# Kernel tuning notes

Hardware: AMD Instinct MI355X
Metric: run time of the kernel (lower is better)

## Reference

```python
import jax, jax.numpy as jnp
import numpy as np

KSIZE = 21
SCALE = 4

def _conv1x1(h, w, b):
    # h: (B, Ci, H, W), w: (Co, Ci), b: (Co,)
    return jnp.einsum('oi,bihw->bohw', w, h) + b[None, :, None, None]

def setup_inputs() -> dict:
    key = jax.random.key(0)
    ks = jax.random.split(key, 8)
    B, C, H, W = 16, 3, 256, 256
    in_nc, nf, nb, K2 = 64, 64, 8, KSIZE * KSIZE
    Hl, Wl = H // SCALE, W // SCALE
    wscale = 0.1
    return {
        'x': jax.random.normal(ks[0], (B, C, H, W), jnp.float32),
        'z': jax.random.normal(ks[1], (B, in_nc, Hl, Wl), jnp.float32),
        'w_in': wscale * jax.random.normal(ks[2], (nf, in_nc), jnp.float32),
        'b_in': jnp.zeros((nf,), jnp.float32),
        'res_w1': wscale * jax.random.normal(ks[3], (nb, nf, nf), jnp.float32),
        'res_b1': jnp.zeros((nb, nf), jnp.float32),
        'res_w2': wscale * jax.random.normal(ks[4], (nb, nf, nf), jnp.float32),
        'res_b2': jnp.zeros((nb, nf), jnp.float32),
        'w_out': wscale * jax.random.normal(ks[5], (K2, nf), jnp.float32),
        'b_out': jnp.zeros((K2,), jnp.float32),
    }

def reference(x, z, w_in, b_in, res_w1, res_b1, res_w2, res_b2, w_out, b_out):
    B, C, H, W = x.shape
    Hl, Wl = z.shape[2], z.shape[3]
    K2 = KSIZE * KSIZE
    pad = KSIZE // 2

    # --- kernel prediction trunk (all 1x1 convs) ---
    h = _conv1x1(z, w_in, b_in)
    for i in range(res_w1.shape[0]):  # fixed n_layers loop
        r = _conv1x1(h, res_w1[i], res_b1[i])
        r = _conv1x1(jax.nn.relu(r), res_w2[i], res_b2[i])
        h = h + r
    logits = _conv1x1(h, w_out, b_out)            # (B, K2, Hl, Wl)
    kernel = jax.nn.softmax(logits, axis=1)       # softmax over kernel taps

    # --- reflection pad + unfold (im2col) with stride=scale ---
    xp = jnp.pad(x, ((0, 0), (0, 0), (pad, pad), (pad, pad)), mode='reflect')
    xr = xp.reshape(B * C, 1, H + 2 * pad, W + 2 * pad)
    patches = jax.lax.conv_general_dilated_patches(
        xr, filter_shape=(KSIZE, KSIZE), window_strides=(SCALE, SCALE),
        padding='VALID', dimension_numbers=('NCHW', 'OIHW', 'NCHW'))
    patches = patches.reshape(B, C, K2, Hl, Wl)   # (B, C, K2, Hl, Wl)

    # --- per-pixel spatially-varying kernel apply ---
    out = (patches * kernel[:, None]).sum(axis=2)  # (B, C, Hl, Wl)
    return out, kernel
```

## Files before the change

### kernel.cpp

```cpp
#include <hip/hip_runtime.h>
#include <math.h>

#define KS 21
#define K2 441
#define NB 8
#define PPI 4096
#define NPIX 65536
#define STR 72
#define XW 276
#define BPX 256
#define NTH 1024
#define XROWS 33
#define XRS 2208
#define LOG2E 1.4426950408889634f

typedef unsigned short u16;
typedef unsigned int u32;
typedef short short8v __attribute__((ext_vector_type(8)));
typedef float f32x4 __attribute__((ext_vector_type(4)));
typedef float f32x16 __attribute__((ext_vector_type(16)));
typedef u32 u32x2v __attribute__((ext_vector_type(2)));

#define WOUT_OFF 69632
#define BOUT_BYTE 196608

#define LDS_HBUF  0
#define LDS_XS    36864
#define LDS_BSH   109728
#define LDS_SBUF  111520
#define LDS_OBUF  113568
#define LDS_TOTAL 119712

#define BAR_LDS()                                                   \
    do {                                                            \
        asm volatile("s_waitcnt lgkmcnt(0)" ::: "memory");          \
        __builtin_amdgcn_s_barrier();                               \
        __builtin_amdgcn_sched_barrier(0);                          \
    } while (0)

__device__ __forceinline__ u16 f2bf(float x)
{
    union { float f; u32 u; } c; c.f = x;
    u32 r = c.u + 0x7FFF + ((c.u >> 16) & 1);
    return (u16)(r >> 16);
}
__device__ __forceinline__ float bflo(u32 w)
{ union { u32 u; float f; } c; c.u = w << 16; return c.f; }
__device__ __forceinline__ float bfhi(u32 w)
{ union { u32 u; float f; } c; c.u = w & 0xffff0000u; return c.f; }

__device__ __forceinline__ int xcd_swz(int i)
{
    return ((i & 7) << 5) | (i >> 3);
}

__device__ __forceinline__ u32 xs_off(int row, int col)
{
    u32 off = (u32)row * XRS + (u32)col * 8;
    return off ^ ((((u32)col >> 4) & 3) << 3);
}

__global__ void prep_kernel(const float* __restrict__ w_in,
                            const float* __restrict__ rw1,
                            const float* __restrict__ rw2,
                            const float* __restrict__ w_out,
                            const float* __restrict__ b_out,
                            u16* __restrict__ wsu, float* __restrict__ bout)
{
    int idx = blockIdx.x * 256 + threadIdx.x;
    if (idx < 69632) {
        int u = idx & 4095;
        int j = u & 7, lane = (u >> 3) & 63, frag = (u >> 9) & 7;
        int kk = frag >> 2, nt = frag & 3, layer = idx >> 12;
        int i = kk * 32 + (lane >> 4) * 8 + j;
        int o = nt * 16 + (lane & 15);
        const float* src;
        if (layer == 0) src = w_in;
        else if (layer & 1) src = rw1 + ((layer - 1) >> 1) * 4096;
        else src = rw2 + ((layer - 2) >> 1) * 4096;
        wsu[idx] = f2bf(src[o * 64 + i]);
    } else if (idx < 69632 + 28672) {
        int u = idx - 69632;
        int j = u & 7, lane = (u >> 3) & 63, t6 = u >> 9;
        int t = t6 % 14, kk = t6 / 14;
        int tap = t * 32 + (lane & 31);
        int i = kk * 16 + (lane >> 5) * 8 + j;
        wsu[idx] = f2bf((tap < K2) ? w_out[tap * 64 + i] * LOG2E : 0.f);
    } else if (idx < 69632 + 28672 + 448) {
        int tap = idx - (69632 + 28672);
        bout[tap] = (tap < K2) ? b_out[tap] * LOG2E : -200.f;
    }
}

__device__ __forceinline__ int reflect256(int v)
{
    v = (v < 0) ? -v : v;
    return (v > 255) ? (510 - v) : v;
}

template <int MODE>
__device__ __forceinline__ void do_layer(u16* hb, const u16* __restrict__ wb,
                                         const float* __restrict__ bias,
                                         float* hreg, int aoff, int wbase,
                                         int c, int g, int lane)
{
    short8v a0 = *(const short8v*)(hb + aoff);
    short8v a1 = *(const short8v*)(hb + aoff + 32);
#pragma unroll
    for (int nt = 0; nt < 4; ++nt) {
        f32x4 acc = {};
        short8v b0 = *(const short8v*)(wb + ((nt)     * 64 + lane) * 8);
        short8v b1 = *(const short8v*)(wb + ((4 + nt) * 64 + lane) * 8);
        acc = __builtin_amdgcn_mfma_f32_16x16x32_bf16(a0, b0, acc, 0, 0, 0);
        acc = __builtin_amdgcn_mfma_f32_16x16x32_bf16(a1, b1, acc, 0, 0, 0);
        const float bv = bias[nt * 16 + c];
#pragma unroll
        for (int r = 0; r < 4; ++r) {
            float v = acc[r] + bv;
            if (MODE == 1) v = fmaxf(v, 0.f);
            if (MODE == 2) { v += hreg[nt * 4 + r]; hreg[nt * 4 + r] = v; }
            if (MODE == 0) hreg[nt * 4 + r] = v;
            hb[(wbase + g * 4 + r) * STR + nt * 16 + c] = f2bf(v);
        }
    }
}

__launch_bounds__(NTH, 1)
__global__ void trunk_kernel(const float* __restrict__ z,
                             const float* __restrict__ x,
                             const float* __restrict__ b_in,
                             const float* __restrict__ rb1,
                             const float* __restrict__ rb2,
                             const u16* __restrict__ wsu,
                             const float* __restrict__ bout,
                             float* __restrict__ out,
                             float* __restrict__ kout)
{
    extern __shared__ __align__(16) char smem[];
    u16*   hbuf = (u16*)(smem + LDS_HBUF);
    char*  xsb  = smem + LDS_XS;
    float* bsh  = (float*)(smem + LDS_BSH);
    float* sbuf = (float*)(smem + LDS_SBUF);
    float* obuf = (float*)(smem + LDS_OBUF);

    const int tid = threadIdx.x, lane = tid & 63, wave = tid >> 6;
    const int pix0 = xcd_swz(blockIdx.x) * BPX;
    const int b = pix0 >> 12, rem0 = pix0 & 4095;
    const int hl0 = rem0 >> 6;

    {
        const int p = tid & 255, i0 = (tid >> 8) * 16;
        const float* zp = z + ((size_t)b * 64 + i0) * PPI + rem0 + p;
        u32* dst = (u32*)hbuf + p * (STR / 2) + i0 / 2;
#pragma unroll
        for (int i = 0; i < 16; i += 2) {
            float v0 = zp[(size_t)i * PPI];
            float v1 = zp[(size_t)(i + 1) * PPI];
            dst[i / 2] = (u32)f2bf(v0) | ((u32)f2bf(v1) << 16);
        }
    }
    for (int u = tid; u < XROWS * XW; u += NTH) {
        int rr = u / XW, c = u - rr * XW;
        int row = reflect256(hl0 * 4 + rr - 10);
        int xcol = reflect256(c - 10);
        const float* xp = x + (size_t)b * 3 * 65536 + row * 256 + xcol;
        u32 w0 = (u32)f2bf(xp[0]) | ((u32)f2bf(xp[65536]) << 16);
        u32 w1 = (u32)f2bf(xp[2 * 65536]);
        u32x2v wv; wv[0] = w0; wv[1] = w1;
        *(u32x2v*)(xsb + xs_off(rr, c)) = wv;
    }
    if (tid < 448) bsh[tid] = bout[tid];
    BAR_LDS();

    const int c16 = lane & 15, g4 = lane >> 4;
    const int wbase = wave * 16;
    const int aoff = (wbase + c16) * STR + g4 * 8;
    float hreg[16];

    do_layer<0>(hbuf, wsu, b_in, hreg, aoff, wbase, c16, g4, lane);
#pragma unroll 1
    for (int l = 0; l < NB; ++l) {
        do_layer<1>(hbuf, wsu + (size_t)(1 + 2 * l) * 4096, rb1 + l * 64,
                    hreg, aoff, wbase, c16, g4, lane);
        do_layer<2>(hbuf, wsu + (size_t)(2 + 2 * l) * 4096, rb2 + l * 64,
                    hreg, aoff, wbase, c16, g4, lane);
    }
    BAR_LDS();

    const int c32 = lane & 31, hi2 = lane >> 5;
    const int wavepx = (wave >> 1) * 32;
    const int tbase = (wave & 1) * 7;

    short8v bh[4];
#pragma unroll
    for (int kk = 0; kk < 4; ++kk)
        bh[kk] = *(const short8v*)(hbuf + (wavepx + c32) * STR + kk * 16 + hi2 * 8);

    float ssum = 0.f;
    u32 epack[56];
    const u16* wob = wsu + WOUT_OFF;
#pragma unroll
    for (int ti = 0; ti < 7; ++ti) {
        const int t = tbase + ti;
        f32x16 acc = {};
#pragma unroll
        for (int kk = 0; kk < 4; ++kk) {
            short8v aw = *(const short8v*)(wob + ((kk * 14 + t) * 64 + lane) * 8);
            acc = __builtin_amdgcn_mfma_f32_32x32x16_bf16(aw, bh[kk], acc, 0, 0, 0);
        }
#pragma unroll
        for (int rr = 0; rr < 8; ++rr) {
            const int r0 = 2 * rr;
            const int tap0 = t * 32 + (r0 & 3) + 8 * (r0 >> 2) + 4 * hi2;
            float e0 = __builtin_amdgcn_exp2f(acc[r0] + bsh[tap0]);
            float e1 = __builtin_amdgcn_exp2f(acc[r0 + 1] + bsh[tap0 + 1]);
            ssum += e0 + e1;
            epack[ti * 8 + rr] = (u32)f2bf(e0) | ((u32)f2bf(e1) << 16);
        }
    }
    ssum += __shfl_xor(ssum, 32);
    if (lane < 32) sbuf[wave * 32 + lane] = ssum;
    BAR_LDS();
    const float inv_s = 1.f / (ssum + sbuf[(wave ^ 1) * 32 + c32]);

    const int pxl = wavepx + c32;
    const int wl = pxl & 63, hlr = pxl >> 6;
    const int xcb4 = wl * 4;
    float* kbase = kout + (size_t)b * K2 * PPI + rem0 + pxl;
    float oacc0 = 0.f, oacc1 = 0.f, oacc2 = 0.f;

#pragma unroll
    for (int ti = 0; ti < 7; ++ti) {
        const int t = tbase + ti;
        int tap = t * 32 + 4 * hi2;
        int ky = tap / KS;
        int kx = tap - ky * KS;
        if (t != 13) {
#pragma unroll
            for (int rr = 0; rr < 8; ++rr) {
                const u32 ep = epack[ti * 8 + rr];
                float p0 = bflo(ep) * inv_s;
                float p1 = bfhi(ep) * inv_s;
                kbase[(size_t)tap * PPI] = p0;
                {
                    u32x2v wv = *(const u32x2v*)(xsb + xs_off(hlr * 4 + ky, xcb4 + kx));
                    oacc0 = fmaf(p0, bflo(wv[0]), oacc0);
                    oacc1 = fmaf(p0, bfhi(wv[0]), oacc1);
                    oacc2 = fmaf(p0, bflo(wv[1]), oacc2);
                }
                tap += 1; kx += 1; if (kx >= KS) { kx -= KS; ky += 1; }
                kbase[(size_t)tap * PPI] = p1;
                {
                    u32x2v wv = *(const u32x2v*)(xsb + xs_off(hlr * 4 + ky, xcb4 + kx));
                    oacc0 = fmaf(p1, bflo(wv[0]), oacc0);
                    oacc1 = fmaf(p1, bfhi(wv[0]), oacc1);
                    oacc2 = fmaf(p1, bflo(wv[1]), oacc2);
                }
                const int d = (rr & 1) ? 5 : 1;
                tap += d; kx += d; if (kx >= KS) { kx -= KS; ky += 1; }
            }
        } else {
#pragma unroll
            for (int rr = 0; rr < 8; ++rr) {
                const u32 ep = epack[ti * 8 + rr];
                float p0 = bflo(ep) * inv_s;
                float p1 = bfhi(ep) * inv_s;
                if (tap < K2) {
                    kbase[(size_t)tap * PPI] = p0;
                    u32x2v wv = *(const u32x2v*)(xsb + xs_off(hlr * 4 + ky, xcb4 + kx));
                    oacc0 = fmaf(p0, bflo(wv[0]), oacc0);
                    oacc1 = fmaf(p0, bfhi(wv[0]), oacc1);
                    oacc2 = fmaf(p0, bflo(wv[1]), oacc2);
                }
                tap += 1; kx += 1; if (kx >= KS) { kx -= KS; ky += 1; }
                if (tap < K2) {
                    kbase[(size_t)tap * PPI] = p1;
                    u32x2v wv = *(const u32x2v*)(xsb + xs_off(hlr * 4 + ky, xcb4 + kx));
                    oacc0 = fmaf(p1, bflo(wv[0]), oacc0);
                    oacc1 = fmaf(p1, bfhi(wv[0]), oacc1);
                    oacc2 = fmaf(p1, bflo(wv[1]), oacc2);
                }
                const int d = (rr & 1) ? 5 : 1;
                tap += d; kx += d; if (kx >= KS) { kx -= KS; ky += 1; }
            }
        }
    }

    oacc0 += __shfl_xor(oacc0, 32);
    oacc1 += __shfl_xor(oacc1, 32);
    oacc2 += __shfl_xor(oacc2, 32);
    if (lane < 32) {
        obuf[(wave * 3 + 0) * 32 + lane] = oacc0;
        obuf[(wave * 3 + 1) * 32 + lane] = oacc1;
        obuf[(wave * 3 + 2) * 32 + lane] = oacc2;
    }
    BAR_LDS();
    if ((wave & 1) == 0 && lane < 32) {
        const int o = rem0 + wavepx + lane;
#pragma unroll
        for (int cch = 0; cch < 3; ++cch) {
            float v = obuf[(wave * 3 + cch) * 32 + lane] +
                      obuf[((wave + 1) * 3 + cch) * 32 + lane];
            out[((size_t)b * 3 + cch) * PPI + o] = v;
        }
    }
}

extern "C" void kernel_launch(void* const* d_in, const int* in_sizes, int n_in,
                              void* d_out, int out_size, void* d_ws, size_t ws_size,
                              hipStream_t stream)
{
    const float* x     = (const float*)d_in[0];
    const float* z     = (const float*)d_in[1];
    const float* w_in  = (const float*)d_in[2];
    const float* b_in  = (const float*)d_in[3];
    const float* rw1   = (const float*)d_in[4];
    const float* rb1   = (const float*)d_in[5];
    const float* rw2   = (const float*)d_in[6];
    const float* rb2   = (const float*)d_in[7];
    const float* w_out = (const float*)d_in[8];
    const float* b_out = (const float*)d_in[9];

    float* out  = (float*)d_out;
    float* kout = out + (size_t)16 * 3 * PPI;
    u16*   wsu  = (u16*)d_ws;
    float* bout = (float*)((char*)d_ws + BOUT_BYTE);

    (void)hipFuncSetAttribute((const void*)trunk_kernel,
                              hipFuncAttributeMaxDynamicSharedMemorySize,
                              LDS_TOTAL);

    prep_kernel<<<(69632 + 28672 + 448 + 255) / 256, 256, 0, stream>>>(
        w_in, rw1, rw2, w_out, b_out, wsu, bout);

    trunk_kernel<<<NPIX / BPX, NTH, LDS_TOTAL, stream>>>(
        z, x, b_in, rb1, rb2, wsu, bout, out, kout);
}
```

Measured before the change: 74.86 us.

## Permute hidden-channel layout in LDS to pack per-lane stores into 8-byte writes

Stores the trunk's hidden activations in LDS with a permuted channel order (chan_of), so each lane's four MFMA output columns are contiguous. Each layer then issues one 8-byte LDS store per row instead of four scalar 2-byte stores. The weight prep and the initial z load are permuted to match, keeping the reduction over channels consistent. This cuts LDS store instruction count in the 17 trunk layers, but the permutation has to stay consistent across every producer and consumer of the hidden buffer.

```diff
diff --git a/kernel.cpp b/kernel.cpp
--- a/kernel.cpp
+++ b/kernel.cpp
@@ -44,6 +44,10 @@
     u32 r = c.u + 0x7FFF + ((c.u >> 16) & 1);
     return (u16)(r >> 16);
 }
+__device__ __forceinline__ u32 pkbf(float a, float b)
+{
+    return (u32)f2bf(a) | ((u32)f2bf(b) << 16);
+}
 __device__ __forceinline__ float bflo(u32 w)
 { union { u32 u; float f; } c; c.u = w << 16; return c.f; }
 __device__ __forceinline__ float bfhi(u32 w)
@@ -52,6 +56,11 @@
 __device__ __forceinline__ int xcd_swz(int i)
 {
     return ((i & 7) << 5) | (i >> 3);
+}
+
+__device__ __forceinline__ int chan_of(int q)
+{
+    return (q & 3) * 16 + (q >> 2);
 }
 
 __device__ __forceinline__ u32 xs_off(int row, int col)
@@ -72,7 +81,8 @@
         int u = idx & 4095;
         int j = u & 7, lane = (u >> 3) & 63, frag = (u >> 9) & 7;
         int kk = frag >> 2, nt = frag & 3, layer = idx >> 12;
-        int i = kk * 32 + (lane >> 4) * 8 + j;
+        int kpos = kk * 32 + (lane >> 4) * 8 + j;
+        int i = chan_of(kpos);
         int o = nt * 16 + (lane & 15);
         const float* src;
         if (layer == 0) src = w_in;
@@ -84,7 +94,8 @@
         int j = u & 7, lane = (u >> 3) & 63, t6 = u >> 9;
         int t = t6 % 14, kk = t6 / 14;
         int tap = t * 32 + (lane & 31);
-        int i = kk * 16 + (lane >> 5) * 8 + j;
+        int kpos = kk * 16 + (lane >> 5) * 8 + j;
+        int i = chan_of(kpos);
         wsu[idx] = f2bf((tap < K2) ? w_out[tap * 64 + i] * LOG2E : 0.f);
     } else if (idx < 69632 + 28672 + 448) {
         int tap = idx - (69632 + 28672);
@@ -106,6 +117,7 @@
 {
     short8v a0 = *(const short8v*)(hb + aoff);
     short8v a1 = *(const short8v*)(hb + aoff + 32);
+    float v[16];
 #pragma unroll
     for (int nt = 0; nt < 4; ++nt) {
         f32x4 acc = {};
@@ -116,12 +128,19 @@
         const float bv = bias[nt * 16 + c];
 #pragma unroll
         for (int r = 0; r < 4; ++r) {
-            float v = acc[r] + bv;
-            if (MODE == 1) v = fmaxf(v, 0.f);
-            if (MODE == 2) { v += hreg[nt * 4 + r]; hreg[nt * 4 + r] = v; }
-            if (MODE == 0) hreg[nt * 4 + r] = v;
-            hb[(wbase + g * 4 + r) * STR + nt * 16 + c] = f2bf(v);
-        }
+            float t = acc[r] + bv;
+            if (MODE == 1) t = fmaxf(t, 0.f);
+            if (MODE == 2) { t += hreg[nt * 4 + r]; hreg[nt * 4 + r] = t; }
+            if (MODE == 0) hreg[nt * 4 + r] = t;
+            v[nt * 4 + r] = t;
+        }
+    }
+#pragma unroll
+    for (int r = 0; r < 4; ++r) {
+        u32x2v wv;
+        wv[0] = pkbf(v[0 * 4 + r], v[1 * 4 + r]);
+        wv[1] = pkbf(v[2 * 4 + r], v[3 * 4 + r]);
+        *(u32x2v*)((char*)hb + ((wbase + g * 4 + r) * STR + c * 4) * 2) = wv;
     }
 }
 
@@ -149,14 +168,17 @@
     const int hl0 = rem0 >> 6;
 
     {
-        const int p = tid & 255, i0 = (tid >> 8) * 16;
-        const float* zp = z + ((size_t)b * 64 + i0) * PPI + rem0 + p;
-        u32* dst = (u32*)hbuf + p * (STR / 2) + i0 / 2;
-#pragma unroll
-        for (int i = 0; i < 16; i += 2) {
-            float v0 = zp[(size_t)i * PPI];
-            float v1 = zp[(size_t)(i + 1) * PPI];
-            dst[i / 2] = (u32)f2bf(v0) | ((u32)f2bf(v1) << 16);
+        const int p = tid & 255, g = tid >> 8;
+        const float* zp = z + (size_t)b * 64 * PPI + rem0 + p;
+        u32* dst = (u32*)hbuf + p * (STR / 2) + g * 8;
+#pragma unroll
+        for (int m = 0; m < 16; m += 2) {
+            int q0 = g * 16 + m;
+            int ch0 = chan_of(q0);
+            int ch1 = chan_of(q0 + 1);
+            float v0 = zp[(size_t)ch0 * PPI];
+            float v1 = zp[(size_t)ch1 * PPI];
+            dst[m / 2] = pkbf(v0, v1);
         }
     }
     for (int u = tid; u < XROWS * XW; u += NTH) {
@@ -164,9 +186,9 @@
         int row = reflect256(hl0 * 4 + rr - 10);
         int xcol = reflect256(c - 10);
         const float* xp = x + (size_t)b * 3 * 65536 + row * 256 + xcol;
-        u32 w0 = (u32)f2bf(xp[0]) | ((u32)f2bf(xp[65536]) << 16);
-        u32 w1 = (u32)f2bf(xp[2 * 65536]);
-        u32x2v wv; wv[0] = w0; wv[1] = w1;
+        u32x2v wv;
+        wv[0] = pkbf(xp[0], xp[65536]);
+        wv[1] = (u32)f2bf(xp[2 * 65536]);
         *(u32x2v*)(xsb + xs_off(rr, c)) = wv;
     }
     if (tid < 448) bsh[tid] = bout[tid];
@@ -215,7 +237,7 @@
             float e0 = __builtin_amdgcn_exp2f(acc[r0] + bsh[tap0]);
             float e1 = __builtin_amdgcn_exp2f(acc[r0 + 1] + bsh[tap0 + 1]);
             ssum += e0 + e1;
-            epack[ti * 8 + rr] = (u32)f2bf(e0) | ((u32)f2bf(e1) << 16);
+            epack[ti * 8 + rr] = pkbf(e0, e1);
         }
     }
     ssum += __shfl_xor(ssum, 32);
```

Result: no change. 75.60 us (+1.0%).
